# Performance work log

Hardware: AMD Instinct MI355X
Metric: run time of the kernel (lower is better)

The kernel has to match this reference:

```python
import jax, jax.numpy as jnp
import numpy as np

BN_EPS = 1e-5


def _lin(x, W, b):
    return x @ W.T + b


def reference(input, first_skeleton, noise, first_W, first_b, gru_Wih, gru_Whh,
              gru_bih, gru_bhh, l0_W, l0_b, res_W, res_b, bn_g, bn_b, bn_m, bn_v,
              fl1_W, fl1_b, fl2_W, fl2_b, fl3_W, fl3_b, qkv_W,
              posm_W1, posm_b1, posm_W2, posm_b2, attn_W1, attn_b1, attn_W2, attn_b2):
    B = input.shape[0]
    # first skeleton embedding -> (B, 50, 1)
    sk = _lin(first_skeleton.reshape(B, 36), first_W, first_b).reshape(B, 50, 1)
    # GRU(10 -> 10), batch_first, h0 = 0
    def gru_step(h, x_t):
        gi = x_t @ gru_Wih.T + gru_bih          # (B, 30)
        gh = h @ gru_Whh.T + gru_bhh
        ir, iz, i_n = jnp.split(gi, 3, axis=-1)
        hr, hz, h_n = jnp.split(gh, 3, axis=-1)
        r = jax.nn.sigmoid(ir + hr)
        z = jax.nn.sigmoid(iz + hz)
        n = jnp.tanh(i_n + r * h_n)
        h_new = (1.0 - z) * n + z * h
        return h_new, h_new
    h0 = jnp.zeros((B, 10), input.dtype)
    _, aux = jax.lax.scan(gru_step, h0, jnp.swapaxes(noise, 0, 1))  # (50, B, 10)
    aux = jnp.tanh(jnp.swapaxes(aux, 0, 1))                          # (B, 50, 10)
    x = jnp.concatenate([input, aux, sk], axis=2).reshape(-1, 267)   # (B*50, 267)
    out = _lin(x, l0_W, l0_b)                                        # (B*50, 1024)
    # three residual Linear+BN(eval)+ReLU blocks
    for i in range(3):
        y = out
        for j in range(2):
            y = _lin(y, res_W[i, j], res_b[i, j])
            y = bn_g[i, j] * (y - bn_m[i, j]) * jax.lax.rsqrt(bn_v[i, j] + BN_EPS) + bn_b[i, j]
            y = jax.nn.relu(y)
        out = y + out
    # dropout: eval mode (identity)
    feats = _lin(out, fl1_W, fl1_b).reshape(B, 50, 128)
    pos = _lin(out, fl2_W, fl2_b).reshape(B, 50, 3)
    # PointTransformerLayer (full attention, mask all True -> no-op)
    qkv = feats @ qkv_W.T                                   # (B, 50, 384)
    q, k, v = jnp.split(qkv, 3, axis=-1)
    rel_pos = pos[:, :, None, :] - pos[:, None, :, :]        # (B, 50, 50, 3)
    rel_emb = _lin(jax.nn.relu(_lin(rel_pos, posm_W1, posm_b1)), posm_W2, posm_b2)  # (B,50,50,128)
    qk_rel = q[:, :, None, :] - k[:, None, :, :]             # (B, 50, 50, 128)
    v_ij = v[:, None, :, :] + rel_emb                        # (B, 50, 50, 128)
    sim = _lin(jax.nn.relu(_lin(qk_rel + rel_emb, attn_W1, attn_b1)), attn_W2, attn_b2)
    attn = jax.nn.softmax(sim, axis=-2)                      # softmax over j
    agg = jnp.einsum('bijd,bijd->bid', attn, v_ij)           # (B, 50, 128)
    o = jnp.tanh(_lin(agg, fl3_W, fl3_b))                    # (B, 50, 36)
    return o


def setup_inputs() -> dict:
    key = jax.random.key(0)
    ks = iter(jax.random.split(key, 64))
    def W(*s):
        return jax.random.normal(next(ks), s, jnp.float32) * 0.02
    B = 256
    z = lambda *s: jnp.zeros(s, jnp.float32)
    return {
        'input': jax.random.normal(next(ks), (B, 50, 256), jnp.float32),
        'first_skeleton': jax.random.normal(next(ks), (B, 36), jnp.float32),
        'noise': jax.random.normal(next(ks), (B, 50, 10), jnp.float32) * 0.33,
        'first_W': W(50, 36), 'first_b': z(50),
        'gru_Wih': W(30, 10), 'gru_Whh': W(30, 10), 'gru_bih': z(30), 'gru_bhh': z(30),
        'l0_W': W(1024, 267), 'l0_b': z(1024),
        'res_W': W(3, 2, 1024, 1024), 'res_b': z(3, 2, 1024),
        'bn_g': jnp.ones((3, 2, 1024), jnp.float32), 'bn_b': z(3, 2, 1024),
        'bn_m': z(3, 2, 1024), 'bn_v': jnp.ones((3, 2, 1024), jnp.float32),
        'fl1_W': W(128, 1024), 'fl1_b': z(128),
        'fl2_W': W(3, 1024), 'fl2_b': z(3),
        'fl3_W': W(36, 128), 'fl3_b': z(36),
        'qkv_W': W(384, 128),
        'posm_W1': W(64, 3), 'posm_b1': z(64), 'posm_W2': W(128, 64), 'posm_b2': z(128),
        'attn_W1': W(512, 128), 'attn_b1': z(512), 'attn_W2': W(128, 512), 'attn_b2': z(128),
    }
```

## Files before the change

### kernel.cpp

```cpp
#include <hip/hip_runtime.h>

typedef __attribute__((ext_vector_type(8))) short bf16x8;
typedef __attribute__((ext_vector_type(4))) float f32x4;
typedef __attribute__((ext_vector_type(4))) ushort u16x4;

__device__ __forceinline__ unsigned f2b2(float lo, float hi) {
    unsigned r;
    asm("v_cvt_pk_bf16_f32 %0, %1, %2" : "=v"(r) : "v"(lo), "v"(hi));
    return r;
}
__device__ __forceinline__ ushort f2b(float v) {
    return (ushort)f2b2(v, v);
}
__device__ __forceinline__ float b2f(ushort b) {
    union { float f; unsigned u; } x; x.u = ((unsigned)b) << 16; return x.f;
}

__device__ __forceinline__ void gl_lds16(const void* g, void* l) {
    __builtin_amdgcn_global_load_lds(
        (__attribute__((address_space(1))) void*)(g),
        (__attribute__((address_space(3))) void*)(l), 16, 0, 0);
}


__global__ void k_split(const float* __restrict__ src, ushort* __restrict__ hi,
                        ushort* __restrict__ lo, int rows, int K, int Kpad) {
    long total = (long)rows * Kpad;
    for (long idx = (long)blockIdx.x * 256 + threadIdx.x; idx < total;
         idx += (long)gridDim.x * 256) {
        int r = (int)(idx / Kpad), c = (int)(idx % Kpad);
        float v = (c < K) ? src[(long)r * K + c] : 0.f;
        ushort h = f2b(v);
        hi[idx] = h;
        if (lo) lo[idx] = f2b(v - b2f(h));
    }
}

__global__ void k_wc(const float* __restrict__ qkvW, const float* __restrict__ fl1W,
                     const float* __restrict__ fl1b, float* __restrict__ Wc,
                     float* __restrict__ bc) {
    int idx = blockIdx.x * 256 + threadIdx.x;
    if (idx >= 384 * 1024) return;
    int n = idx >> 10, k = idx & 1023;
    float s = 0.f;
    #pragma unroll 8
    for (int d = 0; d < 128; ++d) s += qkvW[n * 128 + d] * fl1W[d * 1024 + k];
    Wc[idx] = s;
    if (k == 0) {
        float sb = 0.f;
        #pragma unroll 8
        for (int d = 0; d < 128; ++d) sb += qkvW[n * 128 + d] * fl1b[d];
        bc[n] = sb;
    }
}

__global__ void k_sk(const float* __restrict__ fs, const float* __restrict__ fW,
                     const float* __restrict__ fb, float* __restrict__ sk) {
    int m = blockIdx.x * 256 + threadIdx.x;
    if (m >= 12800) return;
    int b = m / 50, i = m % 50;
    float s = fb[i];
    #pragma unroll 4
    for (int c = 0; c < 36; ++c) s += fs[b * 36 + c] * fW[i * 36 + c];
    sk[m] = s;
}

__global__ void k_gru(const float* __restrict__ noise, const float* __restrict__ Wih,
                      const float* __restrict__ Whh, const float* __restrict__ bih,
                      const float* __restrict__ bhh, float* __restrict__ aux) {
    int lane = threadIdx.x & 63;
    int b = blockIdx.x;
    if (b >= 256) return;
    float wih[10] = {}, whh[10] = {};
    float bi = 0.f, bh = 0.f;
    if (lane < 30) {
        #pragma unroll
        for (int c = 0; c < 10; ++c) { wih[c] = Wih[lane * 10 + c]; whh[c] = Whh[lane * 10 + c]; }
        bi = bih[lane]; bh = bhh[lane];
    }
    float h = 0.f;
    for (int t = 0; t < 50; ++t) {
        float xr = (lane < 10) ? noise[(b * 50 + t) * 10 + lane] : 0.f;
        float gi = bi, gh = bh;
        #pragma unroll
        for (int c = 0; c < 10; ++c) {
            float xc = __shfl(xr, c, 64);
            float hc = __shfl(h, c, 64);
            gi += wih[c] * xc; gh += whh[c] * hc;
        }
        float siz = __shfl(gi, lane + 10, 64), shz = __shfl(gh, lane + 10, 64);
        float sin_ = __shfl(gi, lane + 20, 64), shn = __shfl(gh, lane + 20, 64);
        float r = 1.f / (1.f + expf(-(gi + gh)));
        float z = 1.f / (1.f + expf(-(siz + shz)));
        float n = tanhf(sin_ + r * shn);
        float hn = (1.f - z) * n + z * h;
        if (lane < 10) { h = hn; aux[(b * 50 + t) * 10 + lane] = tanhf(hn); }
    }
}

__global__ void k_xbuild(const float* __restrict__ input, const float* __restrict__ aux,
                         const float* __restrict__ sk, ushort* __restrict__ xhi,
                         long M) {
    long idx = (long)blockIdx.x * 256 + threadIdx.x;
    if (idx >= M * 288) return;
    int m = (int)(idx / 288), c = (int)(idx % 288);
    float v;
    if (c < 256) v = input[(long)m * 256 + c];
    else if (c < 266) v = aux[m * 10 + (c - 256)];
    else if (c == 266) v = sk[m];
    else v = 0.f;
    xhi[idx] = f2b(v);
}

template <int MODE>
__global__ __launch_bounds__(256, 3) void k_gemm(
    const ushort* __restrict__ Ahi,
    const ushort* __restrict__ Bhi,
    int N, int K,
    float* outF, ushort* outHi,
    const float* __restrict__ bias,
    const float* __restrict__ bng, const float* __restrict__ bnb,
    const float* __restrict__ bnm, const float* __restrict__ bnv,
    const ushort* resHi) {
    __shared__ __align__(16) ushort S[2][128][32];
    int t = threadIdx.x;
    int flat = blockIdx.y * gridDim.x + blockIdx.x;
    int nwg = gridDim.x * gridDim.y;
    int q = nwg >> 3, r = nwg & 7;
    int xcd = flat & 7, seq = flat >> 3;
    int wgid = (xcd < r ? xcd * (q + 1) : r * (q + 1) + (xcd - r) * q) + seq;
    int bx = wgid % gridDim.x, by = wgid / gridDim.x;
    int m0 = by * 128, n0 = bx * 128;
    int w = t >> 6, lane = t & 63;
    int wm = w >> 1, wn = w & 1;
    int lo16 = lane & 15, hi4 = lane >> 4;

    const int srow = lane >> 2;
    const int skoff = ((lane & 3) ^ (srow & 3)) * 8;
    const int slot8 = (hi4 ^ (lo16 & 3)) * 8;

    f32x4 acc[4][4];
    #pragma unroll
    for (int i = 0; i < 4; ++i)
        #pragma unroll
        for (int j = 0; j < 4; ++j) acc[i][j] = f32x4{0.f, 0.f, 0.f, 0.f};

    const int nk = K / 32;
    for (int kt = 0; kt < nk; ++kt) {
        const int kb = kt * 32;
        #pragma unroll
        for (int i = 0; i < 2; ++i) {
            int rg = w * 32 + i * 16;
            long ga = (long)(m0 + rg + srow) * K + kb + skoff;
            long gb = (long)(n0 + rg + srow) * K + kb + skoff;
            gl_lds16(&Ahi[ga], &S[0][rg][0]);
            gl_lds16(&Bhi[gb], &S[1][rg][0]);
        }
        __syncthreads();
        bf16x8 ah[4], bh[4];
        #pragma unroll
        for (int m = 0; m < 4; ++m) {
            int row = wm * 64 + m * 16 + lo16;
            ah[m] = *(const bf16x8*)&S[0][row][slot8];
        }
        #pragma unroll
        for (int n = 0; n < 4; ++n) {
            int col = wn * 64 + n * 16 + lo16;
            bh[n] = *(const bf16x8*)&S[1][col][slot8];
        }
        #pragma unroll
        for (int m = 0; m < 4; ++m)
            #pragma unroll
            for (int n = 0; n < 4; ++n)
                acc[m][n] = __builtin_amdgcn_mfma_f32_16x16x32_bf16(ah[m], bh[n], acc[m][n], 0, 0, 0);
        __syncthreads();
    }

    #pragma unroll
    for (int n = 0; n < 4; ++n) {
        int gn = n0 + wn * 64 + n * 16 + lo16;
        float bv = bias ? bias[gn] : 0.f;
        float sc = 1.f, sh = 0.f;
        if (MODE >= 1) { sc = bng[gn] * rsqrtf(bnv[gn] + 1e-5f); sh = bnb[gn] - bnm[gn] * sc; }
        #pragma unroll
        for (int m = 0; m < 4; ++m)
            #pragma unroll
            for (int r2 = 0; r2 < 4; ++r2) {
                int gm = m0 + wm * 64 + m * 16 + hi4 * 4 + r2;
                long o = (long)gm * N + gn;
                float v = acc[m][n][r2] + bv;
                if (MODE >= 1) v = fmaxf(v * sc + sh, 0.f);
                if (MODE == 2) v += b2f(resHi[o]);
                if (outF) outF[o] = v;
                if (outHi) outHi[o] = f2b(v);
            }
    }
}

__global__ void k_fl2(const ushort* __restrict__ hA,
                      const float* __restrict__ W, const float* __restrict__ bias,
                      float* __restrict__ pos) {
    int w = threadIdx.x >> 6, lane = threadIdx.x & 63;
    int m = blockIdx.x * 4 + w;
    float a0 = 0.f, a1 = 0.f, a2 = 0.f;
    for (int k0 = lane * 4; k0 < 1024; k0 += 256) {
        long o = (long)m * 1024 + k0;
        u16x4 hv = *(const u16x4*)&hA[o];
        f32x4 w0 = *(const f32x4*)&W[k0];
        f32x4 w1 = *(const f32x4*)&W[1024 + k0];
        f32x4 w2 = *(const f32x4*)&W[2048 + k0];
        #pragma unroll
        for (int e = 0; e < 4; ++e) {
            float x = b2f(hv[e]);
            a0 += x * w0[e]; a1 += x * w1[e]; a2 += x * w2[e];
        }
    }
    #pragma unroll
    for (int off = 32; off; off >>= 1) {
        a0 += __shfl_xor(a0, off, 64);
        a1 += __shfl_xor(a1, off, 64);
        a2 += __shfl_xor(a2, off, 64);
    }
    if (lane == 0) {
        pos[m * 3 + 0] = a0 + bias[0];
        pos[m * 3 + 1] = a1 + bias[1];
        pos[m * 3 + 2] = a2 + bias[2];
    }
}

__global__ __launch_bounds__(256, 3) void k_attn(
    const float* __restrict__ qkv, const float* __restrict__ posb,
    const ushort* __restrict__ W1b, const ushort* __restrict__ W2b,
    const float* __restrict__ b1, const ushort* __restrict__ pW2b,
    const float* __restrict__ pW1, const float* __restrict__ pb1,
    const float* __restrict__ pb2,
    const float* __restrict__ fl3W, const float* __restrict__ fl3b,
    float* __restrict__ out, long mbase) {
    __shared__ __align__(16) char smem[40960];
    int cpx = gridDim.x >> 3;
    int biL = (blockIdx.x & 7) * cpx + (blockIdx.x >> 3);
    int bL = biL / 50;
    int t = threadIdx.x, w = t >> 6, lane = t & 63;
    int lo16 = lane & 15, hi4 = lane >> 4;

    bf16x8 h_a[2];
    {
        const int jrow = w * 16 + lo16;
        const bool jvalid = jrow < 50;
        float pi0 = posb[biL * 3], pi1 = posb[biL * 3 + 1], pi2 = posb[biL * 3 + 2];
        float d0 = 0.f, d1 = 0.f, d2 = 0.f;
        if (jvalid) {
            int pj = (bL * 50 + jrow) * 3;
            d0 = pi0 - posb[pj]; d1 = pi1 - posb[pj + 1]; d2 = pi2 - posb[pj + 2];
        }
        #pragma unroll
        for (int kt = 0; kt < 2; ++kt) {
            float hv[8];
            #pragma unroll
            for (int e = 0; e < 8; ++e) {
                int ke = kt * 32 + hi4 * 8 + e;
                hv[e] = jvalid
                    ? fmaxf(pb1[ke] + pW1[ke * 3] * d0 + pW1[ke * 3 + 1] * d1
                            + pW1[ke * 3 + 2] * d2, 0.f)
                    : 0.f;
            }
            unsigned* hu = (unsigned*)&h_a[kt];
            #pragma unroll
            for (int i = 0; i < 4; ++i) hu[i] = f2b2(hv[2 * i], hv[2 * i + 1]);
        }
    }

    {
        f32x4 racc[8];
        #pragma unroll
        for (int n = 0; n < 8; ++n) racc[n] = f32x4{0.f, 0.f, 0.f, 0.f};
        #pragma unroll
        for (int kt = 0; kt < 2; ++kt) {
            int k0 = kt * 32 + hi4 * 8;
            #pragma unroll
            for (int n = 0; n < 8; ++n) {
                bf16x8 bv = *(const bf16x8*)&pW2b[(n * 16 + lo16) * 64 + k0];
                racc[n] = __builtin_amdgcn_mfma_f32_16x16x32_bf16(h_a[kt], bv, racc[n], 0, 0, 0);
            }
        }
        int j0 = w * 16 + hi4 * 4;
        #pragma unroll
        for (int n = 0; n < 8; ++n) {
            int col = n * 16 + lo16;
            float pb = pb2[col];
            unsigned p01 = f2b2(racc[n][0] + pb, racc[n][1] + pb);
            unsigned p23 = f2b2(racc[n][2] + pb, racc[n][3] + pb);
            *(ushort*)(smem + (j0 + 0) * 256 + ((col * 2) ^ (((j0 + 0) & 15) << 4))) = (ushort)p01;
            *(ushort*)(smem + (j0 + 1) * 256 + ((col * 2) ^ (((j0 + 1) & 15) << 4))) = (ushort)(p01 >> 16);
            *(ushort*)(smem + (j0 + 2) * 256 + ((col * 2) ^ (((j0 + 2) & 15) << 4))) = (ushort)p23;
            *(ushort*)(smem + (j0 + 3) * 256 + ((col * 2) ^ (((j0 + 3) & 15) << 4))) = (ushort)(p23 >> 16);
        }
    }
    __syncthreads();

    #pragma unroll
    for (int cc = 0; cc < 4; ++cc) {
        int c = cc * 256 + t;
        int row = c >> 4, g = c & 15;
        bf16x8 tv;
        if (row < 50) {
            long kq = (long)biL * 384 + g * 8;
            long kk = (long)(bL * 50 + row) * 384 + 128 + g * 8;
            f32x4 q0 = *(const f32x4*)&qkv[kq];
            f32x4 q1 = *(const f32x4*)&qkv[kq + 4];
            f32x4 k0 = *(const f32x4*)&qkv[kk];
            f32x4 k1 = *(const f32x4*)&qkv[kk + 4];
            bf16x8 rv = *(const bf16x8*)(smem + row * 256 + ((g * 16) ^ ((row & 15) << 4)));
            unsigned* tu = (unsigned*)&tv;
            #pragma unroll
            for (int i = 0; i < 2; ++i)
                tu[i] = f2b2(q0[2 * i] - k0[2 * i] + b2f((ushort)rv[2 * i]),
                             q0[2 * i + 1] - k0[2 * i + 1] + b2f((ushort)rv[2 * i + 1]));
            #pragma unroll
            for (int i = 0; i < 2; ++i)
                tu[2 + i] = f2b2(q1[2 * i] - k1[2 * i] + b2f((ushort)rv[4 + 2 * i]),
                                 q1[2 * i + 1] - k1[2 * i + 1] + b2f((ushort)rv[4 + 2 * i + 1]));
        } else {
            #pragma unroll
            for (int e = 0; e < 8; ++e) tv[e] = 0;
        }
        *(bf16x8*)(smem + 16384 + row * 256 + ((g * 16) ^ ((row & 15) << 4))) = tv;
    }
    __syncthreads();

    f32x4 acc2[4][2];
    #pragma unroll
    for (int m = 0; m < 4; ++m)
        #pragma unroll
        for (int n = 0; n < 2; ++n) acc2[m][n] = f32x4{0.f, 0.f, 0.f, 0.f};

    for (int e8 = 0; e8 < 8; ++e8) {
        f32x4 acc1[4];
        #pragma unroll
        for (int m = 0; m < 4; ++m) acc1[m] = f32x4{0.f, 0.f, 0.f, 0.f};
        __builtin_amdgcn_s_setprio(1);
        #pragma unroll
        for (int kt = 0; kt < 4; ++kt) {
            int col = e8 * 64 + w * 16 + lo16;
            int k = kt * 32 + hi4 * 8;
            bf16x8 bfv = *(const bf16x8*)&W1b[(long)col * 128 + k];
            #pragma unroll
            for (int m = 0; m < 4; ++m) {
                int row = m * 16 + lo16;
                bf16x8 af = *(const bf16x8*)(smem + 16384 + row * 256 +
                          ((k * 2) ^ ((row & 15) << 4)));
                acc1[m] = __builtin_amdgcn_mfma_f32_16x16x32_bf16(af, bfv, acc1[m], 0, 0, 0);
            }
        }
        __builtin_amdgcn_s_setprio(0);
        __syncthreads();
        {
            int ch = w * 16 + lo16;
            float bv = b1[e8 * 64 + ch];
            int row0 = hi4 * 4;
            #pragma unroll
            for (int m = 0; m < 4; ++m) {
                unsigned p01 = f2b2(fmaxf(acc1[m][0] + bv, 0.f), fmaxf(acc1[m][1] + bv, 0.f));
                unsigned p23 = f2b2(fmaxf(acc1[m][2] + bv, 0.f), fmaxf(acc1[m][3] + bv, 0.f));
                int r0 = m * 16 + row0;
                *(ushort*)(smem + 32768 + (r0 + 0) * 128 + ((ch * 2) ^ (((r0 + 0) & 7) << 4))) = (ushort)p01;
                *(ushort*)(smem + 32768 + (r0 + 1) * 128 + ((ch * 2) ^ (((r0 + 1) & 7) << 4))) = (ushort)(p01 >> 16);
                *(ushort*)(smem + 32768 + (r0 + 2) * 128 + ((ch * 2) ^ (((r0 + 2) & 7) << 4))) = (ushort)p23;
                *(ushort*)(smem + 32768 + (r0 + 3) * 128 + ((ch * 2) ^ (((r0 + 3) & 7) << 4))) = (ushort)(p23 >> 16);
            }
        }
        __syncthreads();
        for (int kt2 = 0; kt2 < 2; ++kt2) {
            bf16x8 af[4];
            #pragma unroll
            for (int m = 0; m < 4; ++m) {
                int row = m * 16 + lo16;
                af[m] = *(const bf16x8*)(smem + 32768 + row * 128 +
                          (((kt2 * 32 + hi4 * 8) * 2) ^ ((row & 7) << 4)));
            }
            __builtin_amdgcn_s_setprio(1);
            #pragma unroll
            for (int n = 0; n < 2; ++n) {
                int col = w * 32 + n * 16 + lo16;
                int gk = e8 * 64 + kt2 * 32 + hi4 * 8;
                bf16x8 bfv = *(const bf16x8*)&W2b[(long)col * 512 + gk];
                #pragma unroll
                for (int m = 0; m < 4; ++m)
                    acc2[m][n] = __builtin_amdgcn_mfma_f32_16x16x32_bf16(af[m], bfv, acc2[m][n], 0, 0, 0);
            }
            __builtin_amdgcn_s_setprio(0);
        }
    }

    float outv[2];
    #pragma unroll
    for (int n = 0; n < 2; ++n) {
        float mx = -1e30f;
        #pragma unroll
        for (int m = 0; m < 4; ++m)
            #pragma unroll
            for (int r = 0; r < 4; ++r) {
                int j = m * 16 + hi4 * 4 + r;
                if (j < 50) mx = fmaxf(mx, acc2[m][n][r]);
            }
        mx = fmaxf(mx, __shfl_xor(mx, 16, 64));
        mx = fmaxf(mx, __shfl_xor(mx, 32, 64));
        float e[4][4];
        float sum = 0.f;
        #pragma unroll
        for (int m = 0; m < 4; ++m)
            #pragma unroll
            for (int r = 0; r < 4; ++r) {
                int j = m * 16 + hi4 * 4 + r;
                float ev = (j < 50) ? __expf(acc2[m][n][r] - mx) : 0.f;
                e[m][r] = ev; sum += ev;
            }
        sum += __shfl_xor(sum, 16, 64);
        sum += __shfl_xor(sum, 32, 64);
        float inv = 1.f / sum;
        int col = w * 32 + n * 16 + lo16;
        float ag = 0.f;
        #pragma unroll
        for (int m = 0; m < 4; ++m)
            #pragma unroll
            for (int r = 0; r < 4; ++r) {
                int j = m * 16 + hi4 * 4 + r;
                if (j < 50) {
                    float rl = b2f(*(const ushort*)(smem + j * 256 +
                                  ((col * 2) ^ ((j & 15) << 4))));
                    float vv = qkv[(long)(bL * 50 + j) * 384 + 256 + col] + rl;
                    ag += e[m][r] * inv * vv;
                }
            }
        ag += __shfl_xor(ag, 16, 64);
        ag += __shfl_xor(ag, 32, 64);
        outv[n] = ag;
    }
    float* aggF = (float*)(smem + 16384);
    float* part = (float*)(smem + 16896);
    if (hi4 == 0) {
        aggF[w * 32 + lo16] = outv[0];
        aggF[w * 32 + 16 + lo16] = outv[1];
    }
    if (lane < 36) {
        const float* wf = &fl3W[lane * 128 + w * 32];
        const float* af = aggF + w * 32;
        float s = 0.f;
        #pragma unroll 8
        for (int d = 0; d < 32; ++d) s += af[d] * wf[d];
        part[w * 36 + lane] = s;
    }
    __syncthreads();

    if (t < 36) {
        float s = fl3b[t] + part[t] + part[36 + t] + part[72 + t] + part[108 + t];
        out[(mbase + biL) * 36 + t] = tanhf(s);
    }
}

struct Bufs {
    float *sk, *aux, *qkvF, *posb, *WcF, *bc;
    ushort *xh, *actAh, *actBh;
    ushort *l0Wh, *resWh, *Wch, *aW1b, *aW2b, *pW2b;
};

static size_t plan_ws(char* ws, long MCr, Bufs& B) {
    size_t off = 0;
    auto alloc = [&](size_t n) { char* p = ws + off; off += (n + 255) & ~(size_t)255; return p; };
    B.sk    = (float*) alloc(12800L * 4);
    B.aux   = (float*) alloc(128000L * 4);
    B.xh    = (ushort*)alloc((size_t)MCr * 288 * 2);
    B.actAh = (ushort*)alloc((size_t)MCr * 1024 * 2);
    B.actBh = (ushort*)alloc((size_t)MCr * 1024 * 2);
    B.qkvF  = (float*) alloc((size_t)MCr * 384 * 4);
    B.posb  = (float*) alloc((size_t)MCr * 3 * 4);
    B.l0Wh  = (ushort*)alloc(1024L * 288 * 2);
    B.resWh = (ushort*)alloc(6144L * 1024 * 2);
    B.WcF   = (float*) alloc(384L * 1024 * 4);
    B.Wch   = (ushort*)alloc(384L * 1024 * 2);
    B.bc    = (float*) alloc(384L * 4);
    B.aW1b  = (ushort*)alloc(512L * 128 * 2);
    B.aW2b  = (ushort*)alloc(128L * 512 * 2);
    B.pW2b  = (ushort*)alloc(128L * 64 * 2);
    return off;
}

extern "C" void kernel_launch(void* const* d_in, const int* in_sizes, int n_in,
                              void* d_out, int out_size, void* d_ws, size_t ws_size,
                              hipStream_t stream) {
    (void)in_sizes; (void)n_in;
    const float* input  = (const float*)d_in[0];
    const float* fskel  = (const float*)d_in[1];
    const float* noise  = (const float*)d_in[2];
    const float* firstW = (const float*)d_in[3];
    const float* firstB = (const float*)d_in[4];
    const float* gWih   = (const float*)d_in[5];
    const float* gWhh   = (const float*)d_in[6];
    const float* gbih   = (const float*)d_in[7];
    const float* gbhh   = (const float*)d_in[8];
    const float* l0W    = (const float*)d_in[9];
    const float* l0b    = (const float*)d_in[10];
    const float* resW   = (const float*)d_in[11];
    const float* resB   = (const float*)d_in[12];
    const float* bnG    = (const float*)d_in[13];
    const float* bnB    = (const float*)d_in[14];
    const float* bnM    = (const float*)d_in[15];
    const float* bnV    = (const float*)d_in[16];
    const float* fl1W   = (const float*)d_in[17];
    const float* fl1b   = (const float*)d_in[18];
    const float* fl2W   = (const float*)d_in[19];
    const float* fl2b   = (const float*)d_in[20];
    const float* fl3W   = (const float*)d_in[21];
    const float* fl3b   = (const float*)d_in[22];
    const float* qkvW   = (const float*)d_in[23];
    const float* pW1    = (const float*)d_in[24];
    const float* pb1    = (const float*)d_in[25];
    const float* pW2    = (const float*)d_in[26];
    const float* pb2    = (const float*)d_in[27];
    const float* aW1    = (const float*)d_in[28];
    const float* ab1    = (const float*)d_in[29];
    const float* aW2    = (const float*)d_in[30];
    float* out = (float*)d_out;

    char* ws = (char*)d_ws;
    Bufs B;
    long MCr = 12800;
    if (plan_ws(ws, MCr, B) > ws_size) {
        MCr = 6400;
        if (plan_ws(ws, MCr, B) > ws_size) {
            hipMemsetAsync(d_out, 0, (size_t)out_size * sizeof(float), stream);
            return;
        }
    }
    const int nchunks = (int)(12800 / MCr);

    k_split<<<1152, 256, 0, stream>>>(l0W, B.l0Wh, nullptr, 1024, 267, 288);
    k_split<<<8192, 256, 0, stream>>>(resW, B.resWh, nullptr, 6144, 1024, 1024);
    k_wc<<<1536, 256, 0, stream>>>(qkvW, fl1W, fl1b, B.WcF, B.bc);
    k_split<<<1536, 256, 0, stream>>>(B.WcF, B.Wch, nullptr, 384, 1024, 1024);
    k_split<<<256, 256, 0, stream>>>(aW1, B.aW1b, nullptr, 512, 128, 128);
    k_split<<<256, 256, 0, stream>>>(aW2, B.aW2b, nullptr, 128, 512, 512);
    k_split<<<32, 256, 0, stream>>>(pW2, B.pW2b, nullptr, 128, 64, 64);
    k_sk<<<50, 256, 0, stream>>>(fskel, firstW, firstB, B.sk);
    k_gru<<<256, 64, 0, stream>>>(noise, gWih, gWhh, gbih, gbhh, B.aux);

    for (int c = 0; c < nchunks; ++c) {
        long mbase = (long)c * MCr;
        int xb_grid = (int)((MCr * 288 + 255) / 256);
        k_xbuild<<<xb_grid, 256, 0, stream>>>(input + mbase * 256, B.aux + mbase * 10,
                                              B.sk + mbase, B.xh, MCr);
        dim3 gt(8, (unsigned)(MCr / 128));
        k_gemm<0><<<gt, 256, 0, stream>>>(B.xh, B.l0Wh, 1024, 288,
            nullptr, B.actAh, l0b, nullptr, nullptr, nullptr, nullptr, nullptr);
        for (int blk = 0; blk < 3; ++blk) {
            int j0 = blk * 2, j1 = blk * 2 + 1;
            k_gemm<1><<<gt, 256, 0, stream>>>(B.actAh,
                B.resWh + (size_t)j0 * 1024 * 1024,
                1024, 1024, nullptr, B.actBh, resB + j0 * 1024,
                bnG + j0 * 1024, bnB + j0 * 1024, bnM + j0 * 1024, bnV + j0 * 1024,
                nullptr);
            k_gemm<2><<<gt, 256, 0, stream>>>(B.actBh,
                B.resWh + (size_t)j1 * 1024 * 1024,
                1024, 1024, nullptr, B.actAh, resB + j1 * 1024,
                bnG + j1 * 1024, bnB + j1 * 1024, bnM + j1 * 1024, bnV + j1 * 1024,
                B.actAh);
        }
        dim3 gq(3, (unsigned)(MCr / 128));
        k_gemm<0><<<gq, 256, 0, stream>>>(B.actAh, B.Wch, 384, 1024,
            B.qkvF, nullptr, B.bc, nullptr, nullptr, nullptr, nullptr, nullptr);
        k_fl2<<<(int)(MCr / 4), 256, 0, stream>>>(B.actAh, fl2W, fl2b, B.posb);
        k_attn<<<(int)MCr, 256, 0, stream>>>(B.qkvF, B.posb, B.aW1b, B.aW2b, ab1, B.pW2b,
                                             pW1, pb1, pb2, fl3W, fl3b, out, mbase);
    }
}
```

Baseline: 1.020 ms.

## Split attention into dense-tiled MLP kernel and separate softmax kernel

Moves the per-pair attention MLP into a new kernel that processes 128 flattened (i,j) pairs per block, avoiding the padding of 50 keys up to 64 rows, and stores the logits as fp16 in a workspace buffer. A second kernel recomputes the relative position embedding, then reads the logits to do the softmax, aggregation and output projection. This trades wasted MFMA work for a large extra global write and read, duplicated rel-embedding work, and fp16 rounding of the logits. The workspace fallback now halves the chunk size repeatedly.

```diff
diff --git a/kernel.cpp b/kernel.cpp
--- a/kernel.cpp
+++ b/kernel.cpp
@@ -228,15 +228,196 @@
     }
 }
 
-__global__ __launch_bounds__(256, 3) void k_attn(
+__global__ __launch_bounds__(256, 3) void k_sim(
     const float* __restrict__ qkv, const float* __restrict__ posb,
     const ushort* __restrict__ W1b, const ushort* __restrict__ W2b,
     const float* __restrict__ b1, const ushort* __restrict__ pW2b,
     const float* __restrict__ pW1, const float* __restrict__ pb1,
-    const float* __restrict__ pb2,
+    const float* __restrict__ pb2, _Float16* __restrict__ sim) {
+    __shared__ __align__(16) char smem[49152];
+    int flat = blockIdx.x;
+    int nwg = gridDim.x;
+    int q = nwg >> 3, r = nwg & 7;
+    int xcd = flat & 7, seq = flat >> 3;
+    int wgid = (xcd < r ? xcd * (q + 1) : r * (q + 1) + (xcd - r) * q) + seq;
+    int R0 = wgid * 128;
+    int t = threadIdx.x, w = t >> 6, lane = t & 63;
+    int lo16 = lane & 15, hi4 = lane >> 4;
+    char* H1 = smem + 32768;
+
+    {
+        int rl = t & 127, eh = t >> 7;
+        int g = R0 + rl;
+        int bi = g / 50, j = g - bi * 50;
+        int b = bi / 50;
+        int kv = b * 50 + j;
+        float d0 = posb[bi * 3] - posb[kv * 3];
+        float d1 = posb[bi * 3 + 1] - posb[kv * 3 + 1];
+        float d2 = posb[bi * 3 + 2] - posb[kv * 3 + 2];
+        int swm = (rl & 7) << 4;
+        #pragma unroll
+        for (int e0 = 0; e0 < 32; e0 += 2) {
+            int e = eh * 32 + e0;
+            float v0 = fmaxf(pb1[e] + pW1[e * 3] * d0 + pW1[e * 3 + 1] * d1
+                             + pW1[e * 3 + 2] * d2, 0.f);
+            float v1 = fmaxf(pb1[e + 1] + pW1[e * 3 + 3] * d0 + pW1[e * 3 + 4] * d1
+                             + pW1[e * 3 + 5] * d2, 0.f);
+            *(unsigned*)(H1 + rl * 128 + ((e * 2) ^ swm)) = f2b2(v0, v1);
+        }
+    }
+    __syncthreads();
+
+    {
+        f32x4 racc[8][2];
+        #pragma unroll
+        for (int m = 0; m < 8; ++m)
+            #pragma unroll
+            for (int n = 0; n < 2; ++n) racc[m][n] = f32x4{0.f, 0.f, 0.f, 0.f};
+        #pragma unroll
+        for (int kt = 0; kt < 2; ++kt) {
+            int k0 = kt * 32 + hi4 * 8;
+            bf16x8 bv[2];
+            #pragma unroll
+            for (int n = 0; n < 2; ++n)
+                bv[n] = *(const bf16x8*)&pW2b[(w * 32 + n * 16 + lo16) * 64 + k0];
+            #pragma unroll
+            for (int m = 0; m < 8; ++m) {
+                int row = m * 16 + lo16;
+                bf16x8 ha = *(const bf16x8*)(H1 + row * 128 + ((k0 * 2) ^ ((lo16 & 7) << 4)));
+                #pragma unroll
+                for (int n = 0; n < 2; ++n)
+                    racc[m][n] = __builtin_amdgcn_mfma_f32_16x16x32_bf16(ha, bv[n], racc[m][n], 0, 0, 0);
+            }
+        }
+        #pragma unroll
+        for (int m = 0; m < 8; ++m)
+            #pragma unroll
+            for (int n = 0; n < 2; ++n) {
+                int col = w * 32 + n * 16 + lo16;
+                float pb = pb2[col];
+                #pragma unroll
+                for (int rr = 0; rr < 4; ++rr) {
+                    int row = m * 16 + hi4 * 4 + rr;
+                    *(ushort*)(smem + row * 256 + ((col * 2) ^ ((row & 15) << 4))) =
+                        f2b(racc[m][n][rr] + pb);
+                }
+            }
+    }
+    __syncthreads();
+
+    #pragma unroll
+    for (int cc = 0; cc < 8; ++cc) {
+        int c = cc * 256 + t;
+        int row = c >> 4, g16 = c & 15;
+        int g = R0 + row;
+        int bi = g / 50, j = g - bi * 50;
+        int b = bi / 50;
+        long kq = (long)bi * 384 + g16 * 8;
+        long kk = (long)(b * 50 + j) * 384 + 128 + g16 * 8;
+        f32x4 q0 = *(const f32x4*)&qkv[kq];
+        f32x4 q1 = *(const f32x4*)&qkv[kq + 4];
+        f32x4 k0v = *(const f32x4*)&qkv[kk];
+        f32x4 k1v = *(const f32x4*)&qkv[kk + 4];
+        char* addr = smem + row * 256 + ((g16 * 16) ^ ((row & 15) << 4));
+        bf16x8 rv = *(bf16x8*)addr;
+        bf16x8 tv;
+        unsigned* tu = (unsigned*)&tv;
+        #pragma unroll
+        for (int i = 0; i < 2; ++i)
+            tu[i] = f2b2(q0[2 * i] - k0v[2 * i] + b2f((ushort)rv[2 * i]),
+                         q0[2 * i + 1] - k0v[2 * i + 1] + b2f((ushort)rv[2 * i + 1]));
+        #pragma unroll
+        for (int i = 0; i < 2; ++i)
+            tu[2 + i] = f2b2(q1[2 * i] - k1v[2 * i] + b2f((ushort)rv[4 + 2 * i]),
+                             q1[2 * i + 1] - k1v[2 * i + 1] + b2f((ushort)rv[4 + 2 * i + 1]));
+        *(bf16x8*)addr = tv;
+    }
+    __syncthreads();
+
+    f32x4 acc2[8][2];
+    #pragma unroll
+    for (int m = 0; m < 8; ++m)
+        #pragma unroll
+        for (int n = 0; n < 2; ++n) acc2[m][n] = f32x4{0.f, 0.f, 0.f, 0.f};
+
+    for (int e8 = 0; e8 < 8; ++e8) {
+        f32x4 acc1[8];
+        #pragma unroll
+        for (int m = 0; m < 8; ++m) acc1[m] = f32x4{0.f, 0.f, 0.f, 0.f};
+        __builtin_amdgcn_s_setprio(1);
+        #pragma unroll
+        for (int kt = 0; kt < 4; ++kt) {
+            int col = e8 * 64 + w * 16 + lo16;
+            int k0 = kt * 32 + hi4 * 8;
+            bf16x8 bfv = *(const bf16x8*)&W1b[(long)col * 128 + k0];
+            #pragma unroll
+            for (int m = 0; m < 8; ++m) {
+                int row = m * 16 + lo16;
+                bf16x8 af = *(const bf16x8*)(smem + row * 256 +
+                              ((k0 * 2) ^ ((row & 15) << 4)));
+                acc1[m] = __builtin_amdgcn_mfma_f32_16x16x32_bf16(af, bfv, acc1[m], 0, 0, 0);
+            }
+        }
+        __builtin_amdgcn_s_setprio(0);
+        __syncthreads();
+        {
+            int ch = w * 16 + lo16;
+            float bb = b1[e8 * 64 + ch];
+            #pragma unroll
+            for (int m = 0; m < 8; ++m) {
+                unsigned p01 = f2b2(fmaxf(acc1[m][0] + bb, 0.f), fmaxf(acc1[m][1] + bb, 0.f));
+                unsigned p23 = f2b2(fmaxf(acc1[m][2] + bb, 0.f), fmaxf(acc1[m][3] + bb, 0.f));
+                int r0 = m * 16 + hi4 * 4;
+                *(ushort*)(H1 + (r0 + 0) * 128 + ((ch * 2) ^ (((r0 + 0) & 7) << 4))) = (ushort)p01;
+                *(ushort*)(H1 + (r0 + 1) * 128 + ((ch * 2) ^ (((r0 + 1) & 7) << 4))) = (ushort)(p01 >> 16);
+                *(ushort*)(H1 + (r0 + 2) * 128 + ((ch * 2) ^ (((r0 + 2) & 7) << 4))) = (ushort)p23;
+                *(ushort*)(H1 + (r0 + 3) * 128 + ((ch * 2) ^ (((r0 + 3) & 7) << 4))) = (ushort)(p23 >> 16);
+            }
+        }
+        __syncthreads();
+        #pragma unroll
+        for (int kt2 = 0; kt2 < 2; ++kt2) {
+            int k0 = kt2 * 32 + hi4 * 8;
+            bf16x8 af2[8];
+            #pragma unroll
+            for (int m = 0; m < 8; ++m) {
+                int row = m * 16 + lo16;
+                af2[m] = *(const bf16x8*)(H1 + row * 128 + ((k0 * 2) ^ ((lo16 & 7) << 4)));
+            }
+            __builtin_amdgcn_s_setprio(1);
+            #pragma unroll
+            for (int n = 0; n < 2; ++n) {
+                int col = w * 32 + n * 16 + lo16;
+                bf16x8 w2 = *(const bf16x8*)&W2b[(long)col * 512 + e8 * 64 + k0];
+                #pragma unroll
+                for (int m = 0; m < 8; ++m)
+                    acc2[m][n] = __builtin_amdgcn_mfma_f32_16x16x32_bf16(af2[m], w2, acc2[m][n], 0, 0, 0);
+            }
+            __builtin_amdgcn_s_setprio(0);
+        }
+    }
+
+    #pragma unroll
+    for (int m = 0; m < 8; ++m)
+        #pragma unroll
+        for (int n = 0; n < 2; ++n) {
+            int col = w * 32 + n * 16 + lo16;
+            #pragma unroll
+            for (int rr = 0; rr < 4; ++rr) {
+                int row = m * 16 + hi4 * 4 + rr;
+                sim[(long)(R0 + row) * 128 + col] = (_Float16)acc2[m][n][rr];
+            }
+        }
+}
+
+__global__ __launch_bounds__(256, 3) void k_soft(
+    const float* __restrict__ qkv, const float* __restrict__ posb,
+    const ushort* __restrict__ pW2b,
+    const float* __restrict__ pW1, const float* __restrict__ pb1,
+    const float* __restrict__ pb2, const _Float16* __restrict__ sim,
     const float* __restrict__ fl3W, const float* __restrict__ fl3b,
     float* __restrict__ out, long mbase) {
-    __shared__ __align__(16) char smem[40960];
+    __shared__ __align__(16) char smem[17472];
     int cpx = gridDim.x >> 3;
     int biL = (blockIdx.x & 7) * cpx + (blockIdx.x >> 3);
     int bL = biL / 50;
@@ -298,99 +479,19 @@
     }
     __syncthreads();
 
-    #pragma unroll
-    for (int cc = 0; cc < 4; ++cc) {
-        int c = cc * 256 + t;
-        int row = c >> 4, g = c & 15;
-        bf16x8 tv;
-        if (row < 50) {
-            long kq = (long)biL * 384 + g * 8;
-            long kk = (long)(bL * 50 + row) * 384 + 128 + g * 8;
-            f32x4 q0 = *(const f32x4*)&qkv[kq];
-            f32x4 q1 = *(const f32x4*)&qkv[kq + 4];
-            f32x4 k0 = *(const f32x4*)&qkv[kk];
-            f32x4 k1 = *(const f32x4*)&qkv[kk + 4];
-            bf16x8 rv = *(const bf16x8*)(smem + row * 256 + ((g * 16) ^ ((row & 15) << 4)));
-            unsigned* tu = (unsigned*)&tv;
-            #pragma unroll
-            for (int i = 0; i < 2; ++i)
-                tu[i] = f2b2(q0[2 * i] - k0[2 * i] + b2f((ushort)rv[2 * i]),
-                             q0[2 * i + 1] - k0[2 * i + 1] + b2f((ushort)rv[2 * i + 1]));
-            #pragma unroll
-            for (int i = 0; i < 2; ++i)
-                tu[2 + i] = f2b2(q1[2 * i] - k1[2 * i] + b2f((ushort)rv[4 + 2 * i]),
-                                 q1[2 * i + 1] - k1[2 * i + 1] + b2f((ushort)rv[4 + 2 * i + 1]));
-        } else {
-            #pragma unroll
-            for (int e = 0; e < 8; ++e) tv[e] = 0;
-        }
-        *(bf16x8*)(smem + 16384 + row * 256 + ((g * 16) ^ ((row & 15) << 4))) = tv;
-    }
-    __syncthreads();
-
     f32x4 acc2[4][2];
     #pragma unroll
     for (int m = 0; m < 4; ++m)
         #pragma unroll
-        for (int n = 0; n < 2; ++n) acc2[m][n] = f32x4{0.f, 0.f, 0.f, 0.f};
-
-    for (int e8 = 0; e8 < 8; ++e8) {
-        f32x4 acc1[4];
-        #pragma unroll
-        for (int m = 0; m < 4; ++m) acc1[m] = f32x4{0.f, 0.f, 0.f, 0.f};
-        __builtin_amdgcn_s_setprio(1);
-        #pragma unroll
-        for (int kt = 0; kt < 4; ++kt) {
-            int col = e8 * 64 + w * 16 + lo16;
-            int k = kt * 32 + hi4 * 8;
-            bf16x8 bfv = *(const bf16x8*)&W1b[(long)col * 128 + k];
-            #pragma unroll
-            for (int m = 0; m < 4; ++m) {
-                int row = m * 16 + lo16;
-                bf16x8 af = *(const bf16x8*)(smem + 16384 + row * 256 +
-                          ((k * 2) ^ ((row & 15) << 4)));
-                acc1[m] = __builtin_amdgcn_mfma_f32_16x16x32_bf16(af, bfv, acc1[m], 0, 0, 0);
-            }
-        }
-        __builtin_amdgcn_s_setprio(0);
-        __syncthreads();
-        {
-            int ch = w * 16 + lo16;
-            float bv = b1[e8 * 64 + ch];
-            int row0 = hi4 * 4;
-            #pragma unroll
-            for (int m = 0; m < 4; ++m) {
-                unsigned p01 = f2b2(fmaxf(acc1[m][0] + bv, 0.f), fmaxf(acc1[m][1] + bv, 0.f));
-                unsigned p23 = f2b2(fmaxf(acc1[m][2] + bv, 0.f), fmaxf(acc1[m][3] + bv, 0.f));
-                int r0 = m * 16 + row0;
-                *(ushort*)(smem + 32768 + (r0 + 0) * 128 + ((ch * 2) ^ (((r0 + 0) & 7) << 4))) = (ushort)p01;
-                *(ushort*)(smem + 32768 + (r0 + 1) * 128 + ((ch * 2) ^ (((r0 + 1) & 7) << 4))) = (ushort)(p01 >> 16);
-                *(ushort*)(smem + 32768 + (r0 + 2) * 128 + ((ch * 2) ^ (((r0 + 2) & 7) << 4))) = (ushort)p23;
-                *(ushort*)(smem + 32768 + (r0 + 3) * 128 + ((ch * 2) ^ (((r0 + 3) & 7) << 4))) = (ushort)(p23 >> 16);
-            }
-        }
-        __syncthreads();
-        for (int kt2 = 0; kt2 < 2; ++kt2) {
-            bf16x8 af[4];
-            #pragma unroll
-            for (int m = 0; m < 4; ++m) {
-                int row = m * 16 + lo16;
-                af[m] = *(const bf16x8*)(smem + 32768 + row * 128 +
-                          (((kt2 * 32 + hi4 * 8) * 2) ^ ((row & 7) << 4)));
-            }
-            __builtin_amdgcn_s_setprio(1);
-            #pragma unroll
-            for (int n = 0; n < 2; ++n) {
-                int col = w * 32 + n * 16 + lo16;
-                int gk = e8 * 64 + kt2 * 32 + hi4 * 8;
-                bf16x8 bfv = *(const bf16x8*)&W2b[(long)col * 512 + gk];
-                #pragma unroll
-                for (int m = 0; m < 4; ++m)
-                    acc2[m][n] = __builtin_amdgcn_mfma_f32_16x16x32_bf16(af[m], bfv, acc2[m][n], 0, 0, 0);
-            }
-            __builtin_amdgcn_s_setprio(0);
-        }
-    }
+        for (int n = 0; n < 2; ++n) {
+            int col = w * 32 + n * 16 + lo16;
+            #pragma unroll
+            for (int rr = 0; rr < 4; ++rr) {
+                int j = m * 16 + hi4 * 4 + rr;
+                acc2[m][n][rr] = (j < 50)
+                    ? (float)sim[(long)(biL * 50 + j) * 128 + col] : 0.f;
+            }
+        }
 
     float outv[2];
     #pragma unroll
@@ -399,9 +500,9 @@
         #pragma unroll
         for (int m = 0; m < 4; ++m)
             #pragma unroll
-            for (int r = 0; r < 4; ++r) {
-                int j = m * 16 + hi4 * 4 + r;
-                if (j < 50) mx = fmaxf(mx, acc2[m][n][r]);
+            for (int rr = 0; rr < 4; ++rr) {
+                int j = m * 16 + hi4 * 4 + rr;
+                if (j < 50) mx = fmaxf(mx, acc2[m][n][rr]);
             }
         mx = fmaxf(mx, __shfl_xor(mx, 16, 64));
         mx = fmaxf(mx, __shfl_xor(mx, 32, 64));
@@ -410,10 +511,10 @@
         #pragma unroll
         for (int m = 0; m < 4; ++m)
             #pragma unroll
-            for (int r = 0; r < 4; ++r) {
-                int j = m * 16 + hi4 * 4 + r;
-                float ev = (j < 50) ? __expf(acc2[m][n][r] - mx) : 0.f;
-                e[m][r] = ev; sum += ev;
+            for (int rr = 0; rr < 4; ++rr) {
+                int j = m * 16 + hi4 * 4 + rr;
+                float ev = (j < 50) ? __expf(acc2[m][n][rr] - mx) : 0.f;
+                e[m][rr] = ev; sum += ev;
             }
         sum += __shfl_xor(sum, 16, 64);
         sum += __shfl_xor(sum, 32, 64);
@@ -423,13 +524,13 @@
         #pragma unroll
         for (int m = 0; m < 4; ++m)
             #pragma unroll
-            for (int r = 0; r < 4; ++r) {
-                int j = m * 16 + hi4 * 4 + r;
+            for (int rr = 0; rr < 4; ++rr) {
+                int j = m * 16 + hi4 * 4 + rr;
                 if (j < 50) {
                     float rl = b2f(*(const ushort*)(smem + j * 256 +
                                   ((col * 2) ^ ((j & 15) << 4))));
                     float vv = qkv[(long)(bL * 50 + j) * 384 + 256 + col] + rl;
-                    ag += e[m][r] * inv * vv;
+                    ag += e[m][rr] * inv * vv;
                 }
             }
         ag += __shfl_xor(ag, 16, 64);
@@ -462,6 +563,7 @@
     float *sk, *aux, *qkvF, *posb, *WcF, *bc;
     ushort *xh, *actAh, *actBh;
     ushort *l0Wh, *resWh, *Wch, *aW1b, *aW2b, *pW2b;
+    ushort *sim;
 };
 
 static size_t plan_ws(char* ws, long MCr, Bufs& B) {
@@ -474,6 +576,7 @@
     B.actBh = (ushort*)alloc((size_t)MCr * 1024 * 2);
     B.qkvF  = (float*) alloc((size_t)MCr * 384 * 4);
     B.posb  = (float*) alloc((size_t)MCr * 3 * 4);
+    B.sim   = (ushort*)alloc((size_t)MCr * 50 * 128 * 2);
     B.l0Wh  = (ushort*)alloc(1024L * 288 * 2);
     B.resWh = (ushort*)alloc(6144L * 1024 * 2);
     B.WcF   = (float*) alloc(384L * 1024 * 4);
@@ -525,9 +628,9 @@
     char* ws = (char*)d_ws;
     Bufs B;
     long MCr = 12800;
-    if (plan_ws(ws, MCr, B) > ws_size) {
-        MCr = 6400;
-        if (plan_ws(ws, MCr, B) > ws_size) {
+    while (plan_ws(ws, MCr, B) > ws_size) {
+        MCr >>= 1;
+        if (MCr < 1600) {
             hipMemsetAsync(d_out, 0, (size_t)out_size * sizeof(float), stream);
             return;
         }
@@ -569,7 +672,11 @@
         k_gemm<0><<<gq, 256, 0, stream>>>(B.actAh, B.Wch, 384, 1024,
             B.qkvF, nullptr, B.bc, nullptr, nullptr, nullptr, nullptr, nullptr);
         k_fl2<<<(int)(MCr / 4), 256, 0, stream>>>(B.actAh, fl2W, fl2b, B.posb);
-        k_attn<<<(int)MCr, 256, 0, stream>>>(B.qkvF, B.posb, B.aW1b, B.aW2b, ab1, B.pW2b,
-                                             pW1, pb1, pb2, fl3W, fl3b, out, mbase);
-    }
-}
+        int nsim = (int)(MCr * 50 / 128);
+        k_sim<<<nsim, 256, 0, stream>>>(B.qkvF, B.posb, B.aW1b, B.aW2b, ab1, B.pW2b,
+                                        pW1, pb1, pb2, (_Float16*)B.sim);
+        k_soft<<<(int)MCr, 256, 0, stream>>>(B.qkvF, B.posb, B.pW2b, pW1, pb1, pb2,
+                                             (const _Float16*)B.sim, fl3W, fl3b,
+                                             out, mbase);
+    }
+}
```

Result: faster. 942.1 us (median of 2 runs) (-7.7%).
